# Performance work log

Hardware: AMD Instinct MI355X
Metric: run time of the kernel (lower is better)

The kernel has to match this reference:

```python
import jax, jax.numpy as jnp
import numpy as np

B, S, D = 32, 4096, 64        # batch, n_vec, n_dim
L = 13                        # n_link_all (chord links: 0, 1, 2, 4, ..., 2048)
NW = 13                       # n_W sparse-multiply rounds
HF, HV = 128, 128             # fnet / vnet hidden widths
NC = 2                        # n_class
VOCAB = 512
OFFSETS = [0] + [2 ** k for k in range(L - 1)]  # static python ints


def setup_inputs() -> dict:
    key = jax.random.key(0)
    ks = jax.random.split(key, 8)
    sn = lambda k, shape, sc: (jax.random.normal(k, shape, jnp.float32) * sc)
    return {
        "inputs": jax.random.randint(ks[0], (B, S), 0, VOCAB),
        "emb":  sn(ks[1], (VOCAB, D), 1.0),          # frozen embedding table
        "fW1":  sn(ks[2], (NW, D, HF), 0.1),         # stacked FNet layer-1 weights
        "fb1":  jnp.zeros((NW, HF), jnp.float32),
        "fW2":  sn(ks[3], (NW, HF, L), 0.1),         # stacked FNet layer-2 weights
        "fb2":  jnp.zeros((NW, L), jnp.float32),
        "vW1":  sn(ks[4], (D, HV), 0.1),
        "vb1":  jnp.zeros((HV,), jnp.float32),
        "vW2":  sn(ks[5], (HV, D), 0.1),
        "vb2":  jnp.zeros((D,), jnp.float32),
        "finW": sn(ks[6], (NC, S * D), 0.02),        # torch Linear weight (out, in)
        "finb": jnp.zeros((NC,), jnp.float32),
    }


def _gelu(x):
    return jax.nn.gelu(x, approximate=False)  # torch nn.GELU default (erf)


def reference(inputs, emb, fW1, fb1, fW2, fb2, vW1, vb1, vW2, vb2, finW, finb):
    X = emb[inputs]                                                  # (B,S,D)
    # all NW FNets at once: (NW,B,S,L)
    H = _gelu(jnp.einsum('bsd,kdh->kbsh', X, fW1) + fb1[:, None, None, :])
    Fs = jnp.einsum('kbsh,khl->kbsl', H, fW2) + fb2[:, None, None, :]
    # VNet
    V = _gelu(X @ vW1 + vb1) @ vW2 + vb2                             # (B,S,D)
    # chord sparse multiply rounds with residual:
    # Z[b,i,:] <- sum_l F[b,i,l] * Z[b,(i+off_l) mod S,:]  ;  Z += V
    Z = V
    for k in range(NW):
        Fk = Fs[k]                                                   # (B,S,L)
        Zn = Fk[..., 0][..., None] * Z                               # offset 0
        for l in range(1, L):
            Zn = Zn + Fk[..., l][..., None] * jnp.roll(Z, -OFFSETS[l], axis=1)
        Z = Zn + V
    # NOTE: original source computes logits from V (Z is overwritten); we
    # also return Z so the sparse-multiply loop stays live.
    out = V.reshape(B, S * D) @ finW.T + finb                        # (B,NC)
    return out, Z
```

## Files before the change

### kernel.cpp

```cpp
#include <hip/hip_runtime.h>
#include <hip/hip_bf16.h>
#include <hip/hip_fp16.h>
#include <math.h>

#define S_LEN   4096
#define B_SZ    32
#define D_DIM   64
#define L_LNK   13
#define NW_R    13
#define HF_W    128
#define HV_W    128
#define VOCAB_N 512
#define NC_N    2

#define NT      1024
#define STRIDE  1024
#define NROW    4
#define MIRROR  512
#define BUFN    (S_LEN + MIRROR)

#define ZSCALE     16.0f
#define ZSCALE_INV 0.0625f

typedef float vf4 __attribute__((ext_vector_type(4)));

__device__ __forceinline__ float gelu_erf(float x) {
    return 0.5f * x * (1.0f + erff(x * 0.70710678118654752440f));
}

__device__ __forceinline__ uint2 pack4h(vf4 v) {
    __half2 a = __float22half2_rn(float2{v.x, v.y});
    __half2 b = __float22half2_rn(float2{v.z, v.w});
    uint2 r;
    r.x = *reinterpret_cast<unsigned int*>(&a);
    r.y = *reinterpret_cast<unsigned int*>(&b);
    return r;
}

__device__ __forceinline__ unsigned pk_fma_lo(unsigned c, unsigned z, unsigned a) {
    unsigned d;
    asm("v_pk_fma_f16 %0, %1, %2, %3 op_sel:[0,0,0] op_sel_hi:[0,1,1]"
        : "=v"(d) : "v"(c), "v"(z), "v"(a));
    return d;
}
__device__ __forceinline__ unsigned pk_fma_hi(unsigned c, unsigned z, unsigned a) {
    unsigned d;
    asm("v_pk_fma_f16 %0, %1, %2, %3 op_sel:[1,0,0] op_sel_hi:[1,1,1]"
        : "=v"(d) : "v"(c), "v"(z), "v"(a));
    return d;
}
__device__ __forceinline__ unsigned pk_mul_lo(unsigned c, unsigned z) {
    unsigned d;
    asm("v_pk_mul_f16 %0, %1, %2 op_sel:[0,0] op_sel_hi:[0,1]"
        : "=v"(d) : "v"(c), "v"(z));
    return d;
}
__device__ __forceinline__ unsigned pk_add(unsigned a, unsigned b) {
    unsigned d;
    asm("v_pk_add_f16 %0, %1, %2" : "=v"(d) : "v"(a), "v"(b));
    return d;
}
__device__ __forceinline__ void pk2_lo(uint2& a, unsigned c, uint2 z) {
    a.x = pk_fma_lo(c, z.x, a.x);
    a.y = pk_fma_lo(c, z.y, a.y);
}
__device__ __forceinline__ void pk2_hi(uint2& a, unsigned c, uint2 z) {
    a.x = pk_fma_hi(c, z.x, a.x);
    a.y = pk_fma_hi(c, z.y, a.y);
}

__global__ __launch_bounds__(128)
void tables_kernel(const float* __restrict__ emb,
                   const float* __restrict__ fW1, const float* __restrict__ fb1,
                   const float* __restrict__ fW2, const float* __restrict__ fb2,
                   const float* __restrict__ vW1, const float* __restrict__ vb1,
                   const float* __restrict__ vW2, const float* __restrict__ vb2,
                   __half* __restrict__ F_table, float* __restrict__ V_table) {
    __shared__ float s_emb[D_DIM];
    __shared__ float s_H[HF_W];
    __shared__ float s_red[2][16];
    const int blk = blockIdx.x;
    const int tid = threadIdx.x;

    if (blk < NW_R * VOCAB_N) {
        const int k = blk >> 9;
        const int t = blk & (VOCAB_N - 1);
        if (tid < D_DIM) s_emb[tid] = emb[t * D_DIM + tid];
        __syncthreads();
        float acc = fb1[k * HF_W + tid];
        const float* w = fW1 + (size_t)k * D_DIM * HF_W + tid;
        #pragma unroll 8
        for (int d = 0; d < D_DIM; ++d) acc += s_emb[d] * w[d * HF_W];
        const float hval = gelu_erf(acc);
        const float* w2 = fW2 + ((size_t)k * HF_W + tid) * L_LNK;
        float p[L_LNK];
        #pragma unroll
        for (int l = 0; l < L_LNK; ++l) p[l] = hval * w2[l];
        #pragma unroll
        for (int o = 1; o < 64; o <<= 1) {
            #pragma unroll
            for (int l = 0; l < L_LNK; ++l) p[l] += __shfl_xor(p[l], o, 64);
        }
        if ((tid & 63) == 0) {
            const int wv = tid >> 6;
            #pragma unroll
            for (int l = 0; l < L_LNK; ++l) s_red[wv][l] = p[l];
        }
        __syncthreads();
        if (tid < L_LNK) {
            float o = fb2[k * L_LNK + tid] + s_red[0][tid] + s_red[1][tid];
            F_table[((size_t)(k * VOCAB_N + t)) * 16 + tid] = __float2half_rn(o);
        }
    } else {
        const int t = blk - NW_R * VOCAB_N;
        if (tid < D_DIM) s_emb[tid] = emb[t * D_DIM + tid];
        __syncthreads();
        float acc = vb1[tid];
        const float* w = vW1 + tid;
        #pragma unroll 8
        for (int d = 0; d < D_DIM; ++d) acc += s_emb[d] * w[d * HV_W];
        s_H[tid] = gelu_erf(acc);
        __syncthreads();
        if (tid < D_DIM) {
            float o = vb2[tid];
            const float* w2 = vW2 + tid;
            #pragma unroll 8
            for (int h = 0; h < HV_W; ++h) o += s_H[h] * w2[h * D_DIM];
            V_table[t * D_DIM + tid] = o;
        }
    }
}

__global__ __launch_bounds__(NT, 8)
void chord_kernel(const int* __restrict__ tok,
                  const __half* __restrict__ F_table,
                  const float* __restrict__ V_table,
                  const float* __restrict__ finW,
                  const float* __restrict__ finb,
                  float* __restrict__ out,
                  float* __restrict__ Zout) {
    __shared__ uint2 Zs[2][BUFN];
    __shared__ float slog[16][2];
    const int b = blockIdx.y;
    const int ds = blockIdx.x;
    const int t = threadIdx.x;
    const vf4* V4 = (const vf4*)V_table;

    unsigned tokf[NROW];
    uint2 Vp[NROW], zp[NROW];
    #pragma unroll
    for (int j = 0; j < NROW; ++j) {
        const int r = t + STRIDE * j;
        const int tk = tok[b * S_LEN + r];
        tokf[j] = (unsigned)tk * 32u;
        vf4 v = V4[tk * 16 + ds];
        v.x *= ZSCALE_INV; v.y *= ZSCALE_INV;
        v.z *= ZSCALE_INV; v.w *= ZSCALE_INV;
        uint2 p = pack4h(v);
        Vp[j] = p; zp[j] = p;
        Zs[0][r] = p;
    }
    if (t < MIRROR) Zs[0][S_LEN + t] = zp[0];

    float l0 = 0.0f, l1 = 0.0f;
    {
        const int rb = ds << 8;
        const float4* W0 = (const float4*)finW;
        const float4* W1 = (const float4*)(finW + (size_t)S_LEN * D_DIM);
        const float4* Vt = (const float4*)V_table;
        #pragma unroll
        for (int q = 0; q < 4; ++q) {
            const int i = t + NT * q;
            const int r = rb + (i >> 4);
            const int c4 = i & 15;
            const int tk = tok[b * S_LEN + r];
            float4 v  = Vt[tk * 16 + c4];
            float4 w0 = W0[(size_t)r * 16 + c4];
            float4 w1 = W1[(size_t)r * 16 + c4];
            l0 += v.x * w0.x + v.y * w0.y + v.z * w0.z + v.w * w0.w;
            l1 += v.x * w1.x + v.y * w1.y + v.z * w1.z + v.w * w1.w;
        }
    }
    #pragma unroll
    for (int o = 32; o > 0; o >>= 1) {
        l0 += __shfl_down(l0, o, 64);
        l1 += __shfl_down(l1, o, 64);
    }
    if ((t & 63) == 0) { slog[t >> 6][0] = l0; slog[t >> 6][1] = l1; }
    __syncthreads();
    if (t == 0) {
        float s0 = 0.0f, s1 = 0.0f;
        #pragma unroll
        for (int i = 0; i < 16; ++i) { s0 += slog[i][0]; s1 += slog[i][1]; }
        if (ds == 0) { s0 += finb[0]; s1 += finb[1]; }
        atomicAdd(&out[b * NC_N + 0], s0);
        atomicAdd(&out[b * NC_N + 1], s1);
    }

    int cur = 0;
    uint2 acc[NROW];
    #pragma unroll 1
    for (int k = 0; k < NW_R; ++k) {
        const char* Fk = (const char*)F_table + (size_t)k * (VOCAB_N * 32);
        const uint2* Zc = Zs[cur];
        uint2* Zn = Zs[cur ^ 1];
        const bool wr = (k < NW_R - 1);
        #pragma unroll
        for (int j = 0; j < NROW; ++j) {
            const int r = t + STRIDE * j;
            const char* Fr = Fk + tokf[j];
            uint4 u0 = *(const uint4*)Fr;
            uint4 u1 = *(const uint4*)(Fr + 16);
            uint2 a, a2;
            a.x = pk_fma_lo(u0.x, zp[j].x, Vp[j].x);
            a.y = pk_fma_lo(u0.x, zp[j].y, Vp[j].y);
            {
                uint2 z32 = Zc[r + 32];
                a2.x = pk_mul_lo(u0.w, z32.x);
                a2.y = pk_mul_lo(u0.w, z32.y);
            }
            pk2_hi(a,  u0.x, Zc[r + 1]);
            pk2_lo(a,  u0.y, Zc[r + 2]);
            pk2_hi(a,  u0.y, Zc[r + 4]);
            pk2_lo(a,  u0.z, Zc[r + 8]);
            pk2_hi(a,  u0.z, Zc[r + 16]);
            pk2_hi(a2, u0.w, Zc[r + 64]);
            pk2_lo(a2, u1.x, Zc[r + 128]);
            pk2_hi(a2, u1.x, Zc[r + 256]);
            pk2_lo(a2, u1.y, Zc[r + 512]);
            pk2_hi(a2, u1.y, zp[(j + 1) & 3]);
            pk2_lo(a2, u1.z, zp[(j + 2) & 3]);
            uint2 s;
            s.x = pk_add(a.x, a2.x);
            s.y = pk_add(a.y, a2.y);
            acc[j] = s;
            if (wr) {
                Zn[r] = s;
                if (j == 0 && t < MIRROR) Zn[S_LEN + t] = s;
            }
        }
        if (wr) {
            #pragma unroll
            for (int j = 0; j < NROW; ++j) zp[j] = acc[j];
        }
        __syncthreads();
        cur ^= 1;
    }

    #pragma unroll
    for (int j = 0; j < NROW; ++j) {
        const int r = t + STRIDE * j;
        __half2 h0 = *reinterpret_cast<__half2*>(&acc[j].x);
        __half2 h1 = *reinterpret_cast<__half2*>(&acc[j].y);
        float2 f0 = __half22float2(h0);
        float2 f1 = __half22float2(h1);
        vf4 o;
        o.x = f0.x * ZSCALE; o.y = f0.y * ZSCALE;
        o.z = f1.x * ZSCALE; o.w = f1.y * ZSCALE;
        *(vf4*)(Zout + (((size_t)b * S_LEN + r) << 6) + ds * 4) = o;
    }
}

extern "C" void kernel_launch(void* const* d_in, const int* in_sizes, int n_in,
                              void* d_out, int out_size, void* d_ws, size_t ws_size,
                              hipStream_t stream) {
    const int*   tok  = (const int*)d_in[0];
    const float* emb  = (const float*)d_in[1];
    const float* fW1  = (const float*)d_in[2];
    const float* fb1  = (const float*)d_in[3];
    const float* fW2  = (const float*)d_in[4];
    const float* fb2  = (const float*)d_in[5];
    const float* vW1  = (const float*)d_in[6];
    const float* vb1  = (const float*)d_in[7];
    const float* vW2  = (const float*)d_in[8];
    const float* vb2  = (const float*)d_in[9];
    const float* finW = (const float*)d_in[10];
    const float* finb = (const float*)d_in[11];

    float* out = (float*)d_out;
    float* Z   = out + B_SZ * NC_N;

    float*  V_table = (float*)d_ws;
    __half* F_table = (__half*)(V_table + VOCAB_N * D_DIM);

    tables_kernel<<<NW_R * VOCAB_N + VOCAB_N, 128, 0, stream>>>(
        emb, fW1, fb1, fW2, fb2, vW1, vb1, vW2, vb2, F_table, V_table);
    chord_kernel<<<dim3(16, B_SZ), NT, 0, stream>>>(
        tok, F_table, V_table, finW, finb, out, Z);
}
```

Baseline: 188.3 us.

## Fuse table precompute into chord kernel with a grid-wide atomic barrier

Merges the separate per-token FNet/VNet table kernel into the chord kernel. Each of the 512 blocks computes the tables for one vocabulary token using 8 groups of 128 threads, then all blocks meet at a spin-wait atomic barrier in global memory before the chord rounds. This removes one kernel launch and the gap between the two kernels, but adds a memset and relies on all 512 blocks of 1024 threads being resident at once, with a bounded spin as a fallback.

```diff
diff --git a/kernel.cpp b/kernel.cpp
--- a/kernel.cpp
+++ b/kernel.cpp
@@ -18,6 +18,7 @@
 #define NROW    4
 #define MIRROR  512
 #define BUFN    (S_LEN + MIRROR)
+#define NBLOCKS (16 * B_SZ)
 
 #define ZSCALE     16.0f
 #define ZSCALE_INV 0.0625f
@@ -69,81 +70,99 @@
     a.y = pk_fma_hi(c, z.y, a.y);
 }
 
-__global__ __launch_bounds__(128)
-void tables_kernel(const float* __restrict__ emb,
-                   const float* __restrict__ fW1, const float* __restrict__ fb1,
-                   const float* __restrict__ fW2, const float* __restrict__ fb2,
-                   const float* __restrict__ vW1, const float* __restrict__ vb1,
-                   const float* __restrict__ vW2, const float* __restrict__ vb2,
-                   __half* __restrict__ F_table, float* __restrict__ V_table) {
-    __shared__ float s_emb[D_DIM];
-    __shared__ float s_H[HF_W];
-    __shared__ float s_red[2][16];
-    const int blk = blockIdx.x;
-    const int tid = threadIdx.x;
-
-    if (blk < NW_R * VOCAB_N) {
-        const int k = blk >> 9;
-        const int t = blk & (VOCAB_N - 1);
-        if (tid < D_DIM) s_emb[tid] = emb[t * D_DIM + tid];
-        __syncthreads();
-        float acc = fb1[k * HF_W + tid];
-        const float* w = fW1 + (size_t)k * D_DIM * HF_W + tid;
-        #pragma unroll 8
-        for (int d = 0; d < D_DIM; ++d) acc += s_emb[d] * w[d * HF_W];
-        const float hval = gelu_erf(acc);
-        const float* w2 = fW2 + ((size_t)k * HF_W + tid) * L_LNK;
-        float p[L_LNK];
-        #pragma unroll
-        for (int l = 0; l < L_LNK; ++l) p[l] = hval * w2[l];
-        #pragma unroll
-        for (int o = 1; o < 64; o <<= 1) {
-            #pragma unroll
-            for (int l = 0; l < L_LNK; ++l) p[l] += __shfl_xor(p[l], o, 64);
-        }
-        if ((tid & 63) == 0) {
-            const int wv = tid >> 6;
-            #pragma unroll
-            for (int l = 0; l < L_LNK; ++l) s_red[wv][l] = p[l];
-        }
-        __syncthreads();
-        if (tid < L_LNK) {
-            float o = fb2[k * L_LNK + tid] + s_red[0][tid] + s_red[1][tid];
-            F_table[((size_t)(k * VOCAB_N + t)) * 16 + tid] = __float2half_rn(o);
-        }
-    } else {
-        const int t = blk - NW_R * VOCAB_N;
-        if (tid < D_DIM) s_emb[tid] = emb[t * D_DIM + tid];
-        __syncthreads();
-        float acc = vb1[tid];
-        const float* w = vW1 + tid;
-        #pragma unroll 8
-        for (int d = 0; d < D_DIM; ++d) acc += s_emb[d] * w[d * HV_W];
-        s_H[tid] = gelu_erf(acc);
-        __syncthreads();
-        if (tid < D_DIM) {
-            float o = vb2[tid];
-            const float* w2 = vW2 + tid;
-            #pragma unroll 8
-            for (int h = 0; h < HV_W; ++h) o += s_H[h] * w2[h * D_DIM];
-            V_table[t * D_DIM + tid] = o;
-        }
-    }
-}
-
 __global__ __launch_bounds__(NT, 8)
-void chord_kernel(const int* __restrict__ tok,
-                  const __half* __restrict__ F_table,
-                  const float* __restrict__ V_table,
-                  const float* __restrict__ finW,
-                  const float* __restrict__ finb,
-                  float* __restrict__ out,
-                  float* __restrict__ Zout) {
+void fused_kernel(const int* __restrict__ tok,
+                  const float* __restrict__ emb,
+                  const float* __restrict__ fW1, const float* __restrict__ fb1,
+                  const float* __restrict__ fW2, const float* __restrict__ fb2,
+                  const float* __restrict__ vW1, const float* __restrict__ vb1,
+                  const float* __restrict__ vW2, const float* __restrict__ vb2,
+                  const float* __restrict__ finW, const float* __restrict__ finb,
+                  __half* __restrict__ F_table, float* __restrict__ V_table,
+                  unsigned* __restrict__ bar,
+                  float* __restrict__ out, float* __restrict__ Zout) {
     __shared__ uint2 Zs[2][BUFN];
     __shared__ float slog[16][2];
-    const int b = blockIdx.y;
+    const int b  = blockIdx.y;
     const int ds = blockIdx.x;
-    const int t = threadIdx.x;
+    const int t  = threadIdx.x;
+
+    {
+        const int tkn = b * 16 + ds;
+        float* sf = (float*)&Zs[0][0];
+        float* s_emb = sf;
+        float (*s_red)[2][16] = (float (*)[2][16])(sf + 64);
+        float* s_HV = sf + 64 + 256;
+        const int g = t >> 7;
+        const int u = t & 127;
+
+        if (t < D_DIM) s_emb[t] = emb[tkn * D_DIM + t];
+        __syncthreads();
+
+        #pragma unroll
+        for (int p = 0; p < 2; ++p) {
+            const int unit = g + 8 * p;
+            float pr[L_LNK];
+            if (unit < L_LNK) {
+                const int k = unit;
+                float acc = fb1[k * HF_W + u];
+                const float* w = fW1 + (size_t)k * D_DIM * HF_W + u;
+                #pragma unroll 8
+                for (int d = 0; d < D_DIM; ++d) acc += s_emb[d] * w[d * HF_W];
+                const float hval = gelu_erf(acc);
+                const float* w2 = fW2 + ((size_t)k * HF_W + u) * L_LNK;
+                #pragma unroll
+                for (int l = 0; l < L_LNK; ++l) pr[l] = hval * w2[l];
+                #pragma unroll
+                for (int o = 1; o < 64; o <<= 1) {
+                    #pragma unroll
+                    for (int l = 0; l < L_LNK; ++l) pr[l] += __shfl_xor(pr[l], o, 64);
+                }
+                if ((u & 63) == 0) {
+                    const int wv = u >> 6;
+                    #pragma unroll
+                    for (int l = 0; l < L_LNK; ++l) s_red[g][wv][l] = pr[l];
+                }
+            } else if (unit == 13) {
+                float acc = vb1[u];
+                const float* w = vW1 + u;
+                #pragma unroll 8
+                for (int d = 0; d < D_DIM; ++d) acc += s_emb[d] * w[d * HV_W];
+                s_HV[u] = gelu_erf(acc);
+            }
+            __syncthreads();
+            if (unit < L_LNK) {
+                if (u < L_LNK) {
+                    float o = fb2[unit * L_LNK + u]
+                            + s_red[g][0][u] + s_red[g][1][u];
+                    F_table[((size_t)(unit * VOCAB_N + tkn)) * 16 + u] =
+                        __float2half_rn(o);
+                }
+            } else if (unit == 13 && u < D_DIM) {
+                float o = vb2[u];
+                const float* w2 = vW2 + u;
+                #pragma unroll 8
+                for (int h = 0; h < HV_W; ++h) o += s_HV[h] * w2[h * D_DIM];
+                V_table[tkn * D_DIM + u] = o;
+            }
+            __syncthreads();
+        }
+    }
+
+    __syncthreads();
+    if (t == 0) {
+        __threadfence();
+        __hip_atomic_fetch_add(bar, 1u, __ATOMIC_RELEASE, __HIP_MEMORY_SCOPE_AGENT);
+        unsigned spins = 0;
+        while (__hip_atomic_load(bar, __ATOMIC_ACQUIRE, __HIP_MEMORY_SCOPE_AGENT)
+               < (unsigned)NBLOCKS) {
+            __builtin_amdgcn_s_sleep(2);
+            if (++spins > (1u << 22)) break;
+        }
+        __threadfence();
+    }
+    __syncthreads();
+
     const vf4* V4 = (const vf4*)V_table;
 
     unsigned tokf[NROW];
@@ -280,11 +299,13 @@
     float* out = (float*)d_out;
     float* Z   = out + B_SZ * NC_N;
 
-    float*  V_table = (float*)d_ws;
-    __half* F_table = (__half*)(V_table + VOCAB_N * D_DIM);
-
-    tables_kernel<<<NW_R * VOCAB_N + VOCAB_N, 128, 0, stream>>>(
-        emb, fW1, fb1, fW2, fb2, vW1, vb1, vW2, vb2, F_table, V_table);
-    chord_kernel<<<dim3(16, B_SZ), NT, 0, stream>>>(
-        tok, F_table, V_table, finW, finb, out, Z);
-}
+    float*   V_table = (float*)d_ws;
+    __half*  F_table = (__half*)(V_table + VOCAB_N * D_DIM);
+    unsigned* bar    = (unsigned*)((char*)F_table
+                                   + (size_t)NW_R * VOCAB_N * 16 * sizeof(__half));
+
+    hipMemsetAsync(bar, 0, 8, stream);
+    fused_kernel<<<dim3(16, B_SZ), NT, 0, stream>>>(
+        tok, emb, fW1, fb1, fW2, fb2, vW1, vb1, vW2, vb2, finW, finb,
+        F_table, V_table, bar, out, Z);
+}
```

Result: slower. 264.4 us (+40.4%).
